# Performance work log

Measured on AMD Instinct MI355X. Metric: run time of the kernel, lower is better.

Reference implementation:

```python
import jax, jax.numpy as jnp
import numpy as np
import math

DIM = 512
HEADS = 16
HD = DIM // HEADS
HT, WT = 32, 32          # trained input_resolution
LT = HT * WT             # trained_len
TBL = (2 * HT - 1) * (2 * WT - 1)  # 3969 rows in relative_coords_table
CPB_HID = 512


def _l2norm(a, eps=1e-12):
    n = jnp.linalg.norm(a, axis=-1, keepdims=True)
    return a / jnp.maximum(n, eps)


def setup_inputs() -> dict:
    key = jax.random.key(0)
    ks = jax.random.split(key, 10)
    B, N = 8, 1024
    std = 0.02
    return {
        "x": jax.random.normal(ks[0], (B, N, DIM), jnp.float32),
        "qkv_w": jax.random.normal(ks[1], (3 * DIM, DIM), jnp.float32) * std,
        "qkv_b": jnp.zeros((3 * DIM,), jnp.float32),
        "proj_w": jax.random.normal(ks[2], (DIM, DIM), jnp.float32) * std,
        "proj_b": jnp.zeros((DIM,), jnp.float32),
        # softplus-inverse init: softplus(temperature) == 1/0.24
        "temperature": jnp.log(jnp.exp(jnp.ones((HEADS, 1, 1), jnp.float32) / 0.24) - 1.0),
        "query_embedding": jax.random.normal(ks[3], (HEADS, 1, HD), jnp.float32) * 0.02,
        "cpb_fc1_w": jax.random.normal(ks[4], (CPB_HID, 2), jnp.float32) * std,
        "cpb_fc1_b": jnp.zeros((CPB_HID,), jnp.float32),
        "cpb_fc2_w": jax.random.normal(ks[5], (HEADS, CPB_HID), jnp.float32) * std,
        "cpb_fc2_b": jnp.zeros((HEADS,), jnp.float32),
        "relative_coords_table": jax.random.uniform(ks[6], (TBL, 2), jnp.float32, -1.0, 1.0),
        "relative_pos_index": jax.random.randint(ks[7], (LT * LT,), 0, TBL, jnp.int32),
        "seq_length_scale": jnp.float32(math.log(float(N))),
        "padding_mask": jnp.zeros((B, N), bool),
        "H": 32,
        "W": 32,
    }


def reference(x, qkv_w, qkv_b, proj_w, proj_b, temperature, query_embedding,
              cpb_fc1_w, cpb_fc1_b, cpb_fc2_w, cpb_fc2_b,
              relative_coords_table, seq_length_scale,
              relative_pos_index, padding_mask, H, W):
    B, N, C = x.shape
    # qkv projection -> [B, N, 3, heads, hd] -> per-tensor [B, heads, N, hd]
    qkv = (x @ qkv_w.T + qkv_b).reshape(B, N, 3, HEADS, HD)
    q, k, v = (jnp.transpose(qkv[:, :, i], (0, 2, 1, 3)) for i in range(3))

    # continuous position bias MLP: [TBL, 2] -> [TBL, heads]
    t = jnp.maximum(relative_coords_table @ cpb_fc1_w.T + cpb_fc1_b, 0.0)
    t = t @ cpb_fc2_w.T + cpb_fc2_b                       # [TBL, heads]
    rb = t.T[:, relative_pos_index]                       # [heads, LT*LT]
    rb = rb.reshape(HEADS, LT, HT, WT)
    rb = jax.image.resize(rb, (HEADS, LT, H, W), 'bilinear')   # interp key axis
    rb = rb.reshape(HEADS, LT, N).transpose(0, 2, 1).reshape(HEADS, N, HT, WT)
    rb = jax.image.resize(rb, (HEADS, N, H, W), 'bilinear')    # interp query axis
    rb = rb.reshape(HEADS, N, N).transpose(0, 2, 1)             # [heads, N, N]

    scale = jax.nn.softplus(temperature) * seq_length_scale     # [heads, 1, 1]
    qn = (_l2norm(q) + query_embedding[None]) * scale[None]     # [B, heads, N, hd]
    kn = _l2norm(k)
    attn = jnp.einsum('bhnd,bhmd->bhnm', qn, kn) + rb[None]     # [B, heads, N, N]
    attn = jax.nn.softmax(attn, axis=-1)
    out = jnp.einsum('bhnm,bhmd->bhnd', attn, v)
    out = out.transpose(0, 2, 1, 3).reshape(B, N, C)
    return out @ proj_w.T + proj_b
```

## Files before the change

### kernel.cpp

```cpp
#include <hip/hip_runtime.h>
#include <math.h>

#define BATCH 8
#define NSEQ  1024
#define DIMC  512
#define HEADS 16
#define HD    32
#define TBLN  3969
#define QROWS (BATCH*HEADS*NSEQ)
#define LOG2E 1.4426950408889634f

typedef __attribute__((ext_vector_type(8))) short bf16x8;
typedef __attribute__((ext_vector_type(4))) float f32x4;

__device__ __forceinline__ unsigned short f2bf(float f) {
  union { float f; unsigned u; } c; c.f = f;
  unsigned x = c.u + 0x7fffu + ((c.u >> 16) & 1u);
  return (unsigned short)(x >> 16);
}
__device__ __forceinline__ float bf2f(unsigned short h) {
  union { unsigned u; float f; } c; c.u = ((unsigned)h) << 16; return c.f;
}
__device__ __forceinline__ unsigned cvt_pk_bf16(float lo, float hi) {
  unsigned r;
  asm("v_cvt_pk_bf16_f32 %0, %1, %2" : "=v"(r) : "v"(lo), "v"(hi));
  return r;
}

__global__ __launch_bounds__(256) void split_kernel(
    const float* __restrict__ src, unsigned short* __restrict__ hi,
    unsigned short* __restrict__ lo, int n4)
{
  int gid = blockIdx.x * 256 + threadIdx.x;
  if (gid >= n4) return;
  float4 v = ((const float4*)src)[gid];
  float vv[4] = {v.x, v.y, v.z, v.w};
  unsigned short h[4], l[4];
#pragma unroll
  for (int i = 0; i < 4; ++i) {
    h[i] = f2bf(vv[i]);
    l[i] = f2bf(vv[i] - bf2f(h[i]));
  }
  uint2 hp, lp;
  hp.x = h[0] | ((unsigned)h[1] << 16); hp.y = h[2] | ((unsigned)h[3] << 16);
  lp.x = l[0] | ((unsigned)l[1] << 16); lp.y = l[2] | ((unsigned)l[3] << 16);
  ((uint2*)hi)[gid] = hp;
  ((uint2*)lo)[gid] = lp;
}

template<int EPI>
__global__ __launch_bounds__(256) void gemm_split_kernel(
    const unsigned short* __restrict__ Ah, const unsigned short* __restrict__ Al,
    const unsigned short* __restrict__ Wh, const unsigned short* __restrict__ Wl,
    const float* __restrict__ bias,
    float* __restrict__ o0p, float* __restrict__ o1p, float* __restrict__ o2p)
{
  const int K = DIMC;
  __shared__ __align__(16) unsigned short lds[4 * 4096];
  unsigned short* ldsAh = lds;
  unsigned short* ldsAl = lds + 4096;
  unsigned short* ldsBh = lds + 8192;
  unsigned short* ldsBl = lds + 12288;
  const int tid = threadIdx.x;
  const int wave = tid >> 6, lane = tid & 63;
  const int l16 = lane & 15, hi4 = lane >> 4;
  const int rowBase = blockIdx.y * 128, colBase = blockIdx.x * 128;
  const int warpRow = (wave >> 1) * 64, warpCol = (wave & 1) * 64;

  const int o0 = wave * 2048 + lane * 16;
  const int o1 = o0 + 1024;
  const int row0 = o0 >> 6, s0 = (o0 >> 4) & 3;
  const int row1 = o1 >> 6, s1 = (o1 >> 4) & 3;
  const int g0 = row0 * K + ((s0 ^ ((row0 >> 1) & 3)) << 3);
  const int g1 = row1 * K + ((s1 ^ ((row1 >> 1) & 3)) << 3);

  const unsigned short* A0h = Ah + (size_t)rowBase * K;
  const unsigned short* A0l = Al + (size_t)rowBase * K;
  const unsigned short* W0h = Wh + (size_t)colBase * K;
  const unsigned short* W0l = Wl + (size_t)colBase * K;

  f32x4 acc[4][4] = {};

  float biasv[4];
#pragma unroll
  for (int fj = 0; fj < 4; ++fj)
    biasv[fj] = bias[colBase + warpCol + fj * 16 + l16];

  int ra[4], rbq[4];
#pragma unroll
  for (int f = 0; f < 4; ++f) {
    int rowA = warpRow + f * 16 + l16;
    ra[f] = rowA * 64 + ((hi4 ^ ((rowA >> 1) & 3)) << 4);
    int rowB = warpCol + f * 16 + l16;
    rbq[f] = rowB * 64 + ((hi4 ^ ((rowB >> 1) & 3)) << 4);
  }

#define GLD(gsrc, ldst) __builtin_amdgcn_global_load_lds( \
      (const __attribute__((address_space(1))) unsigned int*)(gsrc), \
      (__attribute__((address_space(3))) unsigned int*)(ldst), 16, 0, 0)

  for (int k0 = 0; k0 < K; k0 += 32) {
    __syncthreads();
    GLD(A0h + k0 + g0, (char*)ldsAh + o0);
    GLD(A0h + k0 + g1, (char*)ldsAh + o1);
    GLD(A0l + k0 + g0, (char*)ldsAl + o0);
    GLD(A0l + k0 + g1, (char*)ldsAl + o1);
    GLD(W0h + k0 + g0, (char*)ldsBh + o0);
    GLD(W0h + k0 + g1, (char*)ldsBh + o1);
    GLD(W0l + k0 + g0, (char*)ldsBl + o0);
    GLD(W0l + k0 + g1, (char*)ldsBl + o1);
    __syncthreads();

    bf16x8 a_h[4], a_l[4], b_h[4], b_l[4];
#pragma unroll
    for (int f = 0; f < 4; ++f) {
      a_h[f] = *(const bf16x8*)((const char*)ldsAh + ra[f]);
      a_l[f] = *(const bf16x8*)((const char*)ldsAl + ra[f]);
      b_h[f] = *(const bf16x8*)((const char*)ldsBh + rbq[f]);
      b_l[f] = *(const bf16x8*)((const char*)ldsBl + rbq[f]);
    }
#pragma unroll
    for (int fi = 0; fi < 4; ++fi)
#pragma unroll
      for (int fj = 0; fj < 4; ++fj) {
        acc[fi][fj] = __builtin_amdgcn_mfma_f32_16x16x32_bf16(a_l[fi], b_h[fj], acc[fi][fj], 0, 0, 0);
        acc[fi][fj] = __builtin_amdgcn_mfma_f32_16x16x32_bf16(a_h[fi], b_l[fj], acc[fi][fj], 0, 0, 0);
        acc[fi][fj] = __builtin_amdgcn_mfma_f32_16x16x32_bf16(a_h[fi], b_h[fj], acc[fi][fj], 0, 0, 0);
      }
  }
#undef GLD

#pragma unroll
  for (int fi = 0; fi < 4; ++fi)
#pragma unroll
    for (int fj = 0; fj < 4; ++fj)
#pragma unroll
      for (int r = 0; r < 4; ++r) {
        int m = rowBase + warpRow + fi * 16 + hi4 * 4 + r;
        int c = colBase + warpCol + fj * 16 + l16;
        float val = acc[fi][fj][r] + biasv[fj];
        if (EPI == 0) {
          int b = m >> 10, n = m & 1023;
          int which = c >> 9, rem = c & 511;
          int hh = rem >> 5, d = rem & 31;
          float* dst = (which == 0) ? o0p : (which == 1) ? o1p : o2p;
          dst[(((size_t)b * HEADS + hh) * NSEQ + n) * HD + d] = val;
        } else {
          o0p[(size_t)m * DIMC + c] = val;
        }
      }
}

__global__ __launch_bounds__(256) void cpb_kernel(
    const float* __restrict__ table, const float* __restrict__ fc1w,
    const float* __restrict__ fc1b, const float* __restrict__ fc2w,
    const float* __restrict__ fc2b, float* __restrict__ tT)
{
  const int row = blockIdx.x;
  const float c0 = table[row*2], c1 = table[row*2+1];
  __shared__ float hid[512];
  __shared__ float red[256];
  const int tid = threadIdx.x;
  for (int j = tid; j < 512; j += 256)
    hid[j] = fmaxf(fmaf(c0, fc1w[j*2], fmaf(c1, fc1w[j*2+1], fc1b[j])), 0.f);
  __syncthreads();
  const int h = tid & 15, part = tid >> 4;
  float s = 0.f;
#pragma unroll
  for (int jj = 0; jj < 32; ++jj) {
    int j = part*32 + jj;
    s = fmaf(hid[j], fc2w[h*512 + j], s);
  }
  red[tid] = s;
  __syncthreads();
  if (tid < 16) {
    float t = fc2b[tid];
#pragma unroll
    for (int p = 0; p < 16; ++p) t += red[tid + p*16];
    tT[(size_t)tid * TBLN + row] = t;
  }
}

__global__ __launch_bounds__(256) void rb_gather_kernel(
    const float* __restrict__ tT, const int* __restrict__ rpi,
    unsigned short* __restrict__ rb)
{
  int gid = blockIdx.x * 256 + threadIdx.x;
  int idx = rpi[gid];
#pragma unroll
  for (int h = 0; h < 16; ++h)
    rb[(size_t)h * NSEQ * NSEQ + gid] = f2bf(tT[h * TBLN + idx] * LOG2E);
}

__global__ __launch_bounds__(256) void rowmax_kernel(
    const unsigned short* __restrict__ rb, float* __restrict__ rbmax)
{
  const int row = blockIdx.x * 4 + (threadIdx.x >> 6);
  const int lane = threadIdx.x & 63;
  const unsigned short* src = rb + (size_t)row * NSEQ + lane * 16;
  bf16x8 a = *(const bf16x8*)src;
  bf16x8 b = *(const bf16x8*)(src + 8);
  float m = -1e30f;
#pragma unroll
  for (int j = 0; j < 8; ++j) {
    m = fmaxf(m, bf2f((unsigned short)a[j]));
    m = fmaxf(m, bf2f((unsigned short)b[j]));
  }
#pragma unroll
  for (int s = 32; s >= 1; s >>= 1) m = fmaxf(m, __shfl_xor(m, s));
  if (lane == 0) rbmax[row] = m;
}

__global__ __launch_bounds__(256) void normsplit_kernel(
    const float* __restrict__ qb, const float* __restrict__ kb,
    const float* __restrict__ temperature, const float* __restrict__ qe,
    const float* __restrict__ sls,
    unsigned short* __restrict__ qh, unsigned short* __restrict__ ql,
    unsigned short* __restrict__ kh, unsigned short* __restrict__ kl,
    float* __restrict__ qmag)
{
  const int gid = blockIdx.x * 256 + threadIdx.x;
  const int lane = gid & 31;
  const int row = gid >> 5;
  const bool isQ = row < QROWS;
  const float* src = isQ ? qb : kb;
  const int r = isQ ? row : row - QROWS;
  float x = src[(size_t)r * HD + lane];
  float ss = x * x;
#pragma unroll
  for (int m = 16; m >= 1; m >>= 1) ss += __shfl_xor(ss, m);
  float y = x / fmaxf(sqrtf(ss), 1e-12f);
  if (isQ) {
    const int h = (r >> 10) & (HEADS - 1);
    float scale = log1pf(__expf(temperature[h])) * sls[0];
    y = (y + qe[h * HD + lane]) * scale;
    float s2 = y * y;
#pragma unroll
    for (int m = 16; m >= 1; m >>= 1) s2 += __shfl_xor(s2, m);
    if (lane == 0) qmag[r] = sqrtf(s2);
  }
  unsigned short hi = f2bf(y);
  unsigned short lo = f2bf(y - bf2f(hi));
  size_t idx = (size_t)r * HD + lane;
  if (isQ) { qh[idx] = hi; ql[idx] = lo; }
  else     { kh[idx] = hi; kl[idx] = lo; }
}

__global__ __launch_bounds__(256) void vt_kernel(
    const float* __restrict__ vb, unsigned short* __restrict__ vt)
{
  __shared__ float tile[32][257];
  const int bh = blockIdx.x, ch = blockIdx.y;
  const int t = threadIdx.x;
  const float* src = vb + ((size_t)bh * NSEQ + ch * 256) * HD;
#pragma unroll
  for (int i = 0; i < 32; ++i) {
    int idx = i * 256 + t;
    tile[idx & 31][idx >> 5] = src[idx];
  }
  __syncthreads();
  unsigned short* dst = vt + (size_t)bh * HD * NSEQ + ch * 256;
#pragma unroll
  for (int i = 0; i < 32; ++i) {
    int idx = i * 256 + t;
    int d = idx >> 8, nl = idx & 255;
    dst[(size_t)d * NSEQ + nl] = f2bf(tile[d][nl]);
  }
}

__global__ __launch_bounds__(256, 4) void attn_mfma_kernel(
    const unsigned short* __restrict__ qh, const unsigned short* __restrict__ ql,
    const unsigned short* __restrict__ kh, const unsigned short* __restrict__ kl,
    const unsigned short* __restrict__ vt, const unsigned short* __restrict__ rb,
    const float* __restrict__ qmag, const float* __restrict__ rbmax,
    unsigned short* __restrict__ aoh, unsigned short* __restrict__ aol)
{
  const int bh = blockIdx.x;
  const int h = bh & (HEADS - 1), b = bh >> 4;
  const int wave = threadIdx.x >> 6;
  const int lane = threadIdx.x & 63;
  const int l16 = lane & 15, hi4 = lane >> 4;
  const int qbase = blockIdx.y * 128 + wave * 32;

  bf16x8 qhf[2], qlf[2];
  float Ms[2];
#pragma unroll
  for (int g = 0; g < 2; ++g) {
    const int qrow = qbase + g * 16 + l16;
    size_t ro = ((size_t)bh * NSEQ + qrow) * HD + hi4 * 8;
    qhf[g] = *(const bf16x8*)(qh + ro);
    qlf[g] = *(const bf16x8*)(ql + ro);
    Ms[g] = qmag[(size_t)bh * NSEQ + qrow] * (1.01f * LOG2E)
            + rbmax[h * NSEQ + qrow] + 0.2f;
  }

  bf16x8 ones;
#pragma unroll
  for (int j = 0; j < 8; ++j) ones[j] = (short)0x3f80;

  f32x4 accV[2][2] = {};
  f32x4 accL[2] = {};

  const int krow_p = 8 * (l16 >> 2) + (l16 & 3);

  for (int kt = 0; kt < NSEQ / 32; ++kt) {
    const int k0 = kt * 32;
    size_t kr0 = ((size_t)bh * NSEQ + k0 + krow_p) * HD + hi4 * 8;
    size_t kr1 = kr0 + 4 * HD;
    bf16x8 kh0 = *(const bf16x8*)(kh + kr0);
    bf16x8 kh1 = *(const bf16x8*)(kh + kr1);
    bf16x8 kl0 = *(const bf16x8*)(kl + kr0);
    bf16x8 kl1 = *(const bf16x8*)(kl + kr1);
    bf16x8 vt0 = *(const bf16x8*)(vt + ((size_t)bh * HD +  0 + l16) * NSEQ + k0 + hi4 * 8);
    bf16x8 vt1 = *(const bf16x8*)(vt + ((size_t)bh * HD + 16 + l16) * NSEQ + k0 + hi4 * 8);

#pragma unroll
    for (int g = 0; g < 2; ++g) {
      f32x4 D0 = {0.f, 0.f, 0.f, 0.f};
      f32x4 D1 = {0.f, 0.f, 0.f, 0.f};
      D0 = __builtin_amdgcn_mfma_f32_16x16x32_bf16(kh0, qhf[g], D0, 0, 0, 0);
      D0 = __builtin_amdgcn_mfma_f32_16x16x32_bf16(kh0, qlf[g], D0, 0, 0, 0);
      D0 = __builtin_amdgcn_mfma_f32_16x16x32_bf16(kl0, qhf[g], D0, 0, 0, 0);
      D1 = __builtin_amdgcn_mfma_f32_16x16x32_bf16(kh1, qhf[g], D1, 0, 0, 0);
      D1 = __builtin_amdgcn_mfma_f32_16x16x32_bf16(kh1, qlf[g], D1, 0, 0, 0);
      D1 = __builtin_amdgcn_mfma_f32_16x16x32_bf16(kl1, qhf[g], D1, 0, 0, 0);

      bf16x8 b8 = *(const bf16x8*)(rb + ((size_t)h * NSEQ + qbase + g * 16 + l16) * NSEQ + k0 + hi4 * 8);

      float p0[4], p1[4];
#pragma unroll
      for (int r = 0; r < 4; ++r) {
        float a0 = fmaf(D0[r], LOG2E, bf2f((unsigned short)b8[r]))     - Ms[g];
        float a1 = fmaf(D1[r], LOG2E, bf2f((unsigned short)b8[4 + r])) - Ms[g];
        p0[r] = __builtin_amdgcn_exp2f(a0);
        p1[r] = __builtin_amdgcn_exp2f(a1);
      }
      union { bf16x8 v; unsigned u[4]; } pa;
      pa.u[0] = cvt_pk_bf16(p0[0], p0[1]);
      pa.u[1] = cvt_pk_bf16(p0[2], p0[3]);
      pa.u[2] = cvt_pk_bf16(p1[0], p1[1]);
      pa.u[3] = cvt_pk_bf16(p1[2], p1[3]);

      accV[g][0] = __builtin_amdgcn_mfma_f32_16x16x32_bf16(pa.v, vt0, accV[g][0], 0, 0, 0);
      accV[g][1] = __builtin_amdgcn_mfma_f32_16x16x32_bf16(pa.v, vt1, accV[g][1], 0, 0, 0);
      accL[g]    = __builtin_amdgcn_mfma_f32_16x16x32_bf16(pa.v, ones, accL[g], 0, 0, 0);
    }
  }

#pragma unroll
  for (int g = 0; g < 2; ++g)
#pragma unroll
    for (int r = 0; r < 4; ++r) {
      float inv = 1.f / accL[g][r];
#pragma unroll
      for (int df = 0; df < 2; ++df) {
        size_t idx = ((size_t)b * NSEQ + qbase + g * 16 + hi4 * 4 + r) * DIMC
                     + h * HD + df * 16 + l16;
        float val = accV[g][df][r] * inv;
        unsigned short hh = f2bf(val);
        aoh[idx] = hh;
        aol[idx] = f2bf(val - bf2f(hh));
      }
    }
}

extern "C" void kernel_launch(void* const* d_in, const int* in_sizes, int n_in,
                              void* d_out, int out_size, void* d_ws, size_t ws_size,
                              hipStream_t stream)
{
  (void)in_sizes; (void)n_in; (void)out_size; (void)ws_size;
  const float* x      = (const float*)d_in[0];
  const float* qkv_w  = (const float*)d_in[1];
  const float* qkv_b  = (const float*)d_in[2];
  const float* proj_w = (const float*)d_in[3];
  const float* proj_b = (const float*)d_in[4];
  const float* temp   = (const float*)d_in[5];
  const float* qe     = (const float*)d_in[6];
  const float* fc1w   = (const float*)d_in[7];
  const float* fc1b   = (const float*)d_in[8];
  const float* fc2w   = (const float*)d_in[9];
  const float* fc2b   = (const float*)d_in[10];
  const float* tbl    = (const float*)d_in[11];
  const int*   rpi    = (const int*)d_in[12];
  const float* sls    = (const float*)d_in[13];

  char* ws = (char*)d_ws;
  const size_t perT = (size_t)BATCH * HEADS * NSEQ * HD;
  float* qb = (float*)ws;
  float* kb = qb + perT;
  float* vb = kb + perT;
  float* tT = vb + perT;
  unsigned short* qh = (unsigned short*)(tT + 65536);
  unsigned short* ql = qh + perT;
  unsigned short* kh = ql + perT;
  unsigned short* kl = kh + perT;
  unsigned short* vt = kl + perT;
  unsigned short* xh = vt + perT;
  unsigned short* xl = xh + perT;
  unsigned short* pwh = xl + perT;
  unsigned short* pwl = pwh + 262144;
  float* rbmax = (float*)(pwl + 262144);
  float* qmag  = rbmax + 16384;
  unsigned short* qwh = qh;
  unsigned short* qwl = qh + 786432;
  unsigned short* rb  = (unsigned short*)qb;
  unsigned short* aoh = xh;
  unsigned short* aol = xl;

  split_kernel<<<dim3(4096), 256, 0, stream>>>(x, xh, xl, 1048576);
  split_kernel<<<dim3(768),  256, 0, stream>>>(qkv_w, qwh, qwl, 196608);
  split_kernel<<<dim3(256),  256, 0, stream>>>(proj_w, pwh, pwl, 65536);
  gemm_split_kernel<0><<<dim3(12, 64), 256, 0, stream>>>(
      xh, xl, qwh, qwl, qkv_b, qb, kb, vb);
  cpb_kernel<<<dim3(TBLN), 256, 0, stream>>>(tbl, fc1w, fc1b, fc2w, fc2b, tT);
  normsplit_kernel<<<dim3((2*QROWS*32)/256), 256, 0, stream>>>(
      qb, kb, temp, qe, sls, qh, ql, kh, kl, qmag);
  vt_kernel<<<dim3(BATCH*HEADS, NSEQ/256), 256, 0, stream>>>(vb, vt);
  rb_gather_kernel<<<dim3((NSEQ*NSEQ)/256), 256, 0, stream>>>(tT, rpi, rb);
  rowmax_kernel<<<dim3(HEADS*NSEQ/4), 256, 0, stream>>>(rb, rbmax);
  attn_mfma_kernel<<<dim3(BATCH*HEADS, NSEQ/128), 256, 0, stream>>>(
      qh, ql, kh, kl, vt, rb, qmag, rbmax, aoh, aol);
  gemm_split_kernel<1><<<dim3(4, 64), 256, 0, stream>>>(
      aoh, aol, pwh, pwl, proj_b, (float*)d_out, nullptr, nullptr);
}
```

Before: 384.0 us.

## Double-buffer K/V/bias tile loads in registers and prioritize MFMA waves in attention

```diff
diff --git a/kernel.cpp b/kernel.cpp
--- a/kernel.cpp
+++ b/kernel.cpp
@@ -26,6 +26,10 @@
   asm("v_cvt_pk_bf16_f32 %0, %1, %2" : "=v"(r) : "v"(lo), "v"(hi));
   return r;
 }
+
+#define GLD(gsrc, ldst) __builtin_amdgcn_global_load_lds( \
+      (const __attribute__((address_space(1))) unsigned int*)(gsrc), \
+      (__attribute__((address_space(3))) unsigned int*)(ldst), 16, 0, 0)
 
 __global__ __launch_bounds__(256) void split_kernel(
     const float* __restrict__ src, unsigned short* __restrict__ hi,
@@ -95,10 +99,6 @@
     rbq[f] = rowB * 64 + ((hi4 ^ ((rowB >> 1) & 3)) << 4);
   }
 
-#define GLD(gsrc, ldst) __builtin_amdgcn_global_load_lds( \
-      (const __attribute__((address_space(1))) unsigned int*)(gsrc), \
-      (__attribute__((address_space(3))) unsigned int*)(ldst), 16, 0, 0)
-
   for (int k0 = 0; k0 < K; k0 += 32) {
     __syncthreads();
     GLD(A0h + k0 + g0, (char*)ldsAh + o0);
@@ -128,7 +128,6 @@
         acc[fi][fj] = __builtin_amdgcn_mfma_f32_16x16x32_bf16(a_h[fi], b_h[fj], acc[fi][fj], 0, 0, 0);
       }
   }
-#undef GLD
 
 #pragma unroll
   for (int fi = 0; fi < 4; ++fi)
@@ -268,7 +267,7 @@
   }
 }
 
-__global__ __launch_bounds__(256, 4) void attn_mfma_kernel(
+__global__ __launch_bounds__(256, 3) void attn_mfma_kernel(
     const unsigned short* __restrict__ qh, const unsigned short* __restrict__ ql,
     const unsigned short* __restrict__ kh, const unsigned short* __restrict__ kl,
     const unsigned short* __restrict__ vt, const unsigned short* __restrict__ rb,
@@ -302,50 +301,72 @@
   f32x4 accL[2] = {};
 
   const int krow_p = 8 * (l16 >> 2) + (l16 & 3);
-
-  for (int kt = 0; kt < NSEQ / 32; ++kt) {
-    const int k0 = kt * 32;
-    size_t kr0 = ((size_t)bh * NSEQ + k0 + krow_p) * HD + hi4 * 8;
-    size_t kr1 = kr0 + 4 * HD;
-    bf16x8 kh0 = *(const bf16x8*)(kh + kr0);
-    bf16x8 kh1 = *(const bf16x8*)(kh + kr1);
-    bf16x8 kl0 = *(const bf16x8*)(kl + kr0);
-    bf16x8 kl1 = *(const bf16x8*)(kl + kr1);
-    bf16x8 vt0 = *(const bf16x8*)(vt + ((size_t)bh * HD +  0 + l16) * NSEQ + k0 + hi4 * 8);
-    bf16x8 vt1 = *(const bf16x8*)(vt + ((size_t)bh * HD + 16 + l16) * NSEQ + k0 + hi4 * 8);
-
-#pragma unroll
-    for (int g = 0; g < 2; ++g) {
-      f32x4 D0 = {0.f, 0.f, 0.f, 0.f};
-      f32x4 D1 = {0.f, 0.f, 0.f, 0.f};
-      D0 = __builtin_amdgcn_mfma_f32_16x16x32_bf16(kh0, qhf[g], D0, 0, 0, 0);
-      D0 = __builtin_amdgcn_mfma_f32_16x16x32_bf16(kh0, qlf[g], D0, 0, 0, 0);
-      D0 = __builtin_amdgcn_mfma_f32_16x16x32_bf16(kl0, qhf[g], D0, 0, 0, 0);
-      D1 = __builtin_amdgcn_mfma_f32_16x16x32_bf16(kh1, qhf[g], D1, 0, 0, 0);
-      D1 = __builtin_amdgcn_mfma_f32_16x16x32_bf16(kh1, qlf[g], D1, 0, 0, 0);
-      D1 = __builtin_amdgcn_mfma_f32_16x16x32_bf16(kl1, qhf[g], D1, 0, 0, 0);
-
-      bf16x8 b8 = *(const bf16x8*)(rb + ((size_t)h * NSEQ + qbase + g * 16 + l16) * NSEQ + k0 + hi4 * 8);
-
-      float p0[4], p1[4];
-#pragma unroll
-      for (int r = 0; r < 4; ++r) {
-        float a0 = fmaf(D0[r], LOG2E, bf2f((unsigned short)b8[r]))     - Ms[g];
-        float a1 = fmaf(D1[r], LOG2E, bf2f((unsigned short)b8[4 + r])) - Ms[g];
-        p0[r] = __builtin_amdgcn_exp2f(a0);
-        p1[r] = __builtin_amdgcn_exp2f(a1);
-      }
-      union { bf16x8 v; unsigned u[4]; } pa;
-      pa.u[0] = cvt_pk_bf16(p0[0], p0[1]);
-      pa.u[1] = cvt_pk_bf16(p0[2], p0[3]);
-      pa.u[2] = cvt_pk_bf16(p1[0], p1[1]);
-      pa.u[3] = cvt_pk_bf16(p1[2], p1[3]);
-
-      accV[g][0] = __builtin_amdgcn_mfma_f32_16x16x32_bf16(pa.v, vt0, accV[g][0], 0, 0, 0);
-      accV[g][1] = __builtin_amdgcn_mfma_f32_16x16x32_bf16(pa.v, vt1, accV[g][1], 0, 0, 0);
-      accL[g]    = __builtin_amdgcn_mfma_f32_16x16x32_bf16(pa.v, ones, accL[g], 0, 0, 0);
-    }
-  }
+  const unsigned short* khg  = kh + ((size_t)bh * NSEQ + krow_p) * HD + hi4 * 8;
+  const unsigned short* klg  = kl + ((size_t)bh * NSEQ + krow_p) * HD + hi4 * 8;
+  const unsigned short* vtg  = vt + ((size_t)bh * HD + l16) * NSEQ + hi4 * 8;
+  const unsigned short* rbg0 = rb + ((size_t)h * NSEQ + qbase + l16) * NSEQ + hi4 * 8;
+  const unsigned short* rbg1 = rbg0 + (size_t)16 * NSEQ;
+
+#define LOADTILE(S, KT) do { \
+    const size_t ko_ = (size_t)(KT) * 32 * HD; \
+    const size_t vo_ = (size_t)(KT) * 32; \
+    kh0##S = *(const bf16x8*)(khg + ko_); \
+    kh1##S = *(const bf16x8*)(khg + ko_ + 4 * HD); \
+    kl0##S = *(const bf16x8*)(klg + ko_); \
+    kl1##S = *(const bf16x8*)(klg + ko_ + 4 * HD); \
+    vt0##S = *(const bf16x8*)(vtg + vo_); \
+    vt1##S = *(const bf16x8*)(vtg + vo_ + (size_t)16 * NSEQ); \
+    b80##S = *(const bf16x8*)(rbg0 + vo_); \
+    b81##S = *(const bf16x8*)(rbg1 + vo_); \
+  } while (0)
+
+#define COMPUTE(S) do { \
+    _Pragma("unroll") \
+    for (int g = 0; g < 2; ++g) { \
+      bf16x8 b8v = g ? b81##S : b80##S; \
+      f32x4 D0 = {0.f, 0.f, 0.f, 0.f}; \
+      f32x4 D1 = {0.f, 0.f, 0.f, 0.f}; \
+      __builtin_amdgcn_s_setprio(1); \
+      D0 = __builtin_amdgcn_mfma_f32_16x16x32_bf16(kh0##S, qhf[g], D0, 0, 0, 0); \
+      D0 = __builtin_amdgcn_mfma_f32_16x16x32_bf16(kh0##S, qlf[g], D0, 0, 0, 0); \
+      D0 = __builtin_amdgcn_mfma_f32_16x16x32_bf16(kl0##S, qhf[g], D0, 0, 0, 0); \
+      D1 = __builtin_amdgcn_mfma_f32_16x16x32_bf16(kh1##S, qhf[g], D1, 0, 0, 0); \
+      D1 = __builtin_amdgcn_mfma_f32_16x16x32_bf16(kh1##S, qlf[g], D1, 0, 0, 0); \
+      D1 = __builtin_amdgcn_mfma_f32_16x16x32_bf16(kl1##S, qhf[g], D1, 0, 0, 0); \
+      __builtin_amdgcn_s_setprio(0); \
+      float p0[4], p1[4]; \
+      _Pragma("unroll") \
+      for (int r = 0; r < 4; ++r) { \
+        float a0 = fmaf(D0[r], LOG2E, bf2f((unsigned short)b8v[r]))     - Ms[g]; \
+        float a1 = fmaf(D1[r], LOG2E, bf2f((unsigned short)b8v[4 + r])) - Ms[g]; \
+        p0[r] = __builtin_amdgcn_exp2f(a0); \
+        p1[r] = __builtin_amdgcn_exp2f(a1); \
+      } \
+      union { bf16x8 v; unsigned u[4]; } pa; \
+      pa.u[0] = cvt_pk_bf16(p0[0], p0[1]); \
+      pa.u[1] = cvt_pk_bf16(p0[2], p0[3]); \
+      pa.u[2] = cvt_pk_bf16(p1[0], p1[1]); \
+      pa.u[3] = cvt_pk_bf16(p1[2], p1[3]); \
+      __builtin_amdgcn_s_setprio(1); \
+      accV[g][0] = __builtin_amdgcn_mfma_f32_16x16x32_bf16(pa.v, vt0##S, accV[g][0], 0, 0, 0); \
+      accV[g][1] = __builtin_amdgcn_mfma_f32_16x16x32_bf16(pa.v, vt1##S, accV[g][1], 0, 0, 0); \
+      accL[g]    = __builtin_amdgcn_mfma_f32_16x16x32_bf16(pa.v, ones, accL[g], 0, 0, 0); \
+      __builtin_amdgcn_s_setprio(0); \
+    } \
+  } while (0)
+
+  bf16x8 kh0A, kh1A, kl0A, kl1A, vt0A, vt1A, b80A, b81A;
+  bf16x8 kh0B, kh1B, kl0B, kl1B, vt0B, vt1B, b80B, b81B;
+
+  LOADTILE(A, 0);
+  for (int kt = 0; kt < 32; kt += 2) {
+    LOADTILE(B, kt + 1);
+    COMPUTE(A);
+    LOADTILE(A, kt + 2);
+    COMPUTE(B);
+  }
+#undef LOADTILE
+#undef COMPUTE
 
 #pragma unroll
   for (int g = 0; g < 2; ++g)
```

New measurement: 388.1 us. About the same (+1.1%).

## Pre-swizzle K, V and bias into MFMA fragment layout for coalesced attention loads

Applied to the files above, without the earlier changes.

```diff
diff --git a/kernel.cpp b/kernel.cpp
--- a/kernel.cpp
+++ b/kernel.cpp
@@ -26,6 +26,10 @@
   asm("v_cvt_pk_bf16_f32 %0, %1, %2" : "=v"(r) : "v"(lo), "v"(hi));
   return r;
 }
+
+#define GLD(gsrc, ldst) __builtin_amdgcn_global_load_lds( \
+      (const __attribute__((address_space(1))) unsigned int*)(gsrc), \
+      (__attribute__((address_space(3))) unsigned int*)(ldst), 16, 0, 0)
 
 __global__ __launch_bounds__(256) void split_kernel(
     const float* __restrict__ src, unsigned short* __restrict__ hi,
@@ -95,10 +99,6 @@
     rbq[f] = rowB * 64 + ((hi4 ^ ((rowB >> 1) & 3)) << 4);
   }
 
-#define GLD(gsrc, ldst) __builtin_amdgcn_global_load_lds( \
-      (const __attribute__((address_space(1))) unsigned int*)(gsrc), \
-      (__attribute__((address_space(3))) unsigned int*)(ldst), 16, 0, 0)
-
   for (int k0 = 0; k0 < K; k0 += 32) {
     __syncthreads();
     GLD(A0h + k0 + g0, (char*)ldsAh + o0);
@@ -128,7 +128,6 @@
         acc[fi][fj] = __builtin_amdgcn_mfma_f32_16x16x32_bf16(a_h[fi], b_h[fj], acc[fi][fj], 0, 0, 0);
       }
   }
-#undef GLD
 
 #pragma unroll
   for (int fi = 0; fi < 4; ++fi)
@@ -183,23 +182,36 @@
 
 __global__ __launch_bounds__(256) void rb_gather_kernel(
     const float* __restrict__ tT, const int* __restrict__ rpi,
-    unsigned short* __restrict__ rb)
+    unsigned short* __restrict__ rbT)
 {
   int gid = blockIdx.x * 256 + threadIdx.x;
-  int idx = rpi[gid];
-#pragma unroll
-  for (int h = 0; h < 16; ++h)
-    rb[(size_t)h * NSEQ * NSEQ + gid] = f2bf(tT[h * TBLN + idx] * LOG2E);
+  int n = gid >> 7, m8 = gid & 127;
+  int idx[8];
+#pragma unroll
+  for (int j = 0; j < 8; ++j) idx[j] = rpi[(size_t)n * NSEQ + m8 * 8 + j];
+  const int kt = m8 >> 2, hi4v = m8 & 3;
+  const size_t base = (((size_t)0 * 64 + (n >> 4)) * 32 + kt) * 512
+                      + ((n & 15) + 16 * hi4v) * 8;
+#pragma unroll
+  for (int h = 0; h < 16; ++h) {
+    bf16x8 v;
+#pragma unroll
+    for (int j = 0; j < 8; ++j)
+      v[j] = (short)f2bf(tT[h * TBLN + idx[j]] * LOG2E);
+    *(bf16x8*)(rbT + base + (size_t)h * 64 * 32 * 512) = v;
+  }
 }
 
 __global__ __launch_bounds__(256) void rowmax_kernel(
-    const unsigned short* __restrict__ rb, float* __restrict__ rbmax)
+    const unsigned short* __restrict__ rbT, float* __restrict__ rbmax)
 {
   const int row = blockIdx.x * 4 + (threadIdx.x >> 6);
   const int lane = threadIdx.x & 63;
-  const unsigned short* src = rb + (size_t)row * NSEQ + lane * 16;
-  bf16x8 a = *(const bf16x8*)src;
-  bf16x8 b = *(const bf16x8*)(src + 8);
+  const int h = row >> 10, n = row & 1023;
+  const int kt = lane >> 1, half = lane & 1;
+  const size_t base = (((size_t)h * 64 + (n >> 4)) * 32 + kt) * 512;
+  bf16x8 a = *(const bf16x8*)(rbT + base + ((n & 15) + 16 * (2 * half)) * 8);
+  bf16x8 b = *(const bf16x8*)(rbT + base + ((n & 15) + 16 * (2 * half + 1)) * 8);
   float m = -1e30f;
 #pragma unroll
   for (int j = 0; j < 8; ++j) {
@@ -216,7 +228,7 @@
     const float* __restrict__ temperature, const float* __restrict__ qe,
     const float* __restrict__ sls,
     unsigned short* __restrict__ qh, unsigned short* __restrict__ ql,
-    unsigned short* __restrict__ kh, unsigned short* __restrict__ kl,
+    unsigned short* __restrict__ khT, unsigned short* __restrict__ klT,
     float* __restrict__ qmag)
 {
   const int gid = blockIdx.x * 256 + threadIdx.x;
@@ -241,13 +253,22 @@
   }
   unsigned short hi = f2bf(y);
   unsigned short lo = f2bf(y - bf2f(hi));
-  size_t idx = (size_t)r * HD + lane;
-  if (isQ) { qh[idx] = hi; ql[idx] = lo; }
-  else     { kh[idx] = hi; kl[idx] = lo; }
+  if (isQ) {
+    size_t idx = (size_t)r * HD + lane;
+    qh[idx] = hi; ql[idx] = lo;
+  } else {
+    const int bh = r >> 10, n = r & 1023;
+    const int kt = n >> 5, kr = n & 31;
+    const int s = (kr >> 2) & 1;
+    const int l16v = 4 * (kr >> 3) + (kr & 3);
+    size_t idx = ((((size_t)bh * 32 + kt) * 2 + s) * 512)
+                 + (l16v + 16 * (lane >> 3)) * 8 + (lane & 7);
+    khT[idx] = hi; klT[idx] = lo;
+  }
 }
 
 __global__ __launch_bounds__(256) void vt_kernel(
-    const float* __restrict__ vb, unsigned short* __restrict__ vt)
+    const float* __restrict__ vb, unsigned short* __restrict__ vtT)
 {
   __shared__ float tile[32][257];
   const int bh = blockIdx.x, ch = blockIdx.y;
@@ -259,19 +280,22 @@
     tile[idx & 31][idx >> 5] = src[idx];
   }
   __syncthreads();
-  unsigned short* dst = vt + (size_t)bh * HD * NSEQ + ch * 256;
+  unsigned short* dst = vtT + (size_t)bh * 32 * 2 * 512;
 #pragma unroll
   for (int i = 0; i < 32; ++i) {
     int idx = i * 256 + t;
     int d = idx >> 8, nl = idx & 255;
-    dst[(size_t)d * NSEQ + nl] = f2bf(tile[d][nl]);
-  }
-}
-
-__global__ __launch_bounds__(256, 4) void attn_mfma_kernel(
+    int n = ch * 256 + nl;
+    size_t a = (((size_t)(n >> 5) * 2) + (d >> 4)) * 512
+               + ((d & 15) + 16 * ((n >> 3) & 3)) * 8 + (n & 7);
+    dst[a] = f2bf(tile[d][nl]);
+  }
+}
+
+__global__ __launch_bounds__(256, 6) void attn_mfma_kernel(
     const unsigned short* __restrict__ qh, const unsigned short* __restrict__ ql,
-    const unsigned short* __restrict__ kh, const unsigned short* __restrict__ kl,
-    const unsigned short* __restrict__ vt, const unsigned short* __restrict__ rb,
+    const unsigned short* __restrict__ khT, const unsigned short* __restrict__ klT,
+    const unsigned short* __restrict__ vtT, const unsigned short* __restrict__ rbT,
     const float* __restrict__ qmag, const float* __restrict__ rbmax,
     unsigned short* __restrict__ aoh, unsigned short* __restrict__ aol)
 {
@@ -280,88 +304,84 @@
   const int wave = threadIdx.x >> 6;
   const int lane = threadIdx.x & 63;
   const int l16 = lane & 15, hi4 = lane >> 4;
-  const int qbase = blockIdx.y * 128 + wave * 32;
-
-  bf16x8 qhf[2], qlf[2];
-  float Ms[2];
-#pragma unroll
-  for (int g = 0; g < 2; ++g) {
-    const int qrow = qbase + g * 16 + l16;
+  const int qbase = blockIdx.y * 64 + wave * 16;
+
+  const int qrow = qbase + l16;
+  bf16x8 qhf, qlf;
+  {
     size_t ro = ((size_t)bh * NSEQ + qrow) * HD + hi4 * 8;
-    qhf[g] = *(const bf16x8*)(qh + ro);
-    qlf[g] = *(const bf16x8*)(ql + ro);
-    Ms[g] = qmag[(size_t)bh * NSEQ + qrow] * (1.01f * LOG2E)
-            + rbmax[h * NSEQ + qrow] + 0.2f;
-  }
+    qhf = *(const bf16x8*)(qh + ro);
+    qlf = *(const bf16x8*)(ql + ro);
+  }
+  const float Ms = qmag[(size_t)bh * NSEQ + qrow] * (1.01f * LOG2E)
+                   + rbmax[h * NSEQ + qrow] + 0.2f;
 
   bf16x8 ones;
 #pragma unroll
   for (int j = 0; j < 8; ++j) ones[j] = (short)0x3f80;
 
-  f32x4 accV[2][2] = {};
-  f32x4 accL[2] = {};
-
-  const int krow_p = 8 * (l16 >> 2) + (l16 & 3);
-
-  for (int kt = 0; kt < NSEQ / 32; ++kt) {
-    const int k0 = kt * 32;
-    size_t kr0 = ((size_t)bh * NSEQ + k0 + krow_p) * HD + hi4 * 8;
-    size_t kr1 = kr0 + 4 * HD;
-    bf16x8 kh0 = *(const bf16x8*)(kh + kr0);
-    bf16x8 kh1 = *(const bf16x8*)(kh + kr1);
-    bf16x8 kl0 = *(const bf16x8*)(kl + kr0);
-    bf16x8 kl1 = *(const bf16x8*)(kl + kr1);
-    bf16x8 vt0 = *(const bf16x8*)(vt + ((size_t)bh * HD +  0 + l16) * NSEQ + k0 + hi4 * 8);
-    bf16x8 vt1 = *(const bf16x8*)(vt + ((size_t)bh * HD + 16 + l16) * NSEQ + k0 + hi4 * 8);
-
-#pragma unroll
-    for (int g = 0; g < 2; ++g) {
-      f32x4 D0 = {0.f, 0.f, 0.f, 0.f};
-      f32x4 D1 = {0.f, 0.f, 0.f, 0.f};
-      D0 = __builtin_amdgcn_mfma_f32_16x16x32_bf16(kh0, qhf[g], D0, 0, 0, 0);
-      D0 = __builtin_amdgcn_mfma_f32_16x16x32_bf16(kh0, qlf[g], D0, 0, 0, 0);
-      D0 = __builtin_amdgcn_mfma_f32_16x16x32_bf16(kl0, qhf[g], D0, 0, 0, 0);
-      D1 = __builtin_amdgcn_mfma_f32_16x16x32_bf16(kh1, qhf[g], D1, 0, 0, 0);
-      D1 = __builtin_amdgcn_mfma_f32_16x16x32_bf16(kh1, qlf[g], D1, 0, 0, 0);
-      D1 = __builtin_amdgcn_mfma_f32_16x16x32_bf16(kl1, qhf[g], D1, 0, 0, 0);
-
-      bf16x8 b8 = *(const bf16x8*)(rb + ((size_t)h * NSEQ + qbase + g * 16 + l16) * NSEQ + k0 + hi4 * 8);
-
-      float p0[4], p1[4];
-#pragma unroll
-      for (int r = 0; r < 4; ++r) {
-        float a0 = fmaf(D0[r], LOG2E, bf2f((unsigned short)b8[r]))     - Ms[g];
-        float a1 = fmaf(D1[r], LOG2E, bf2f((unsigned short)b8[4 + r])) - Ms[g];
-        p0[r] = __builtin_amdgcn_exp2f(a0);
-        p1[r] = __builtin_amdgcn_exp2f(a1);
-      }
-      union { bf16x8 v; unsigned u[4]; } pa;
-      pa.u[0] = cvt_pk_bf16(p0[0], p0[1]);
-      pa.u[1] = cvt_pk_bf16(p0[2], p0[3]);
-      pa.u[2] = cvt_pk_bf16(p1[0], p1[1]);
-      pa.u[3] = cvt_pk_bf16(p1[2], p1[3]);
-
-      accV[g][0] = __builtin_amdgcn_mfma_f32_16x16x32_bf16(pa.v, vt0, accV[g][0], 0, 0, 0);
-      accV[g][1] = __builtin_amdgcn_mfma_f32_16x16x32_bf16(pa.v, vt1, accV[g][1], 0, 0, 0);
-      accL[g]    = __builtin_amdgcn_mfma_f32_16x16x32_bf16(pa.v, ones, accL[g], 0, 0, 0);
+  f32x4 accV0 = {}, accV1 = {}, accL = {};
+
+  const unsigned short* khB = khT + (size_t)bh * 32768 + lane * 8;
+  const unsigned short* klB = klT + (size_t)bh * 32768 + lane * 8;
+  const unsigned short* vtB = vtT + (size_t)bh * 32768 + lane * 8;
+  const unsigned short* rbB = rbT
+      + ((size_t)(h * 64 + blockIdx.y * 4 + wave) * 32) * 512 + lane * 8;
+
+  for (int kt = 0; kt < 32; ++kt) {
+    bf16x8 kh0 = *(const bf16x8*)(khB + kt * 1024);
+    bf16x8 kh1 = *(const bf16x8*)(khB + kt * 1024 + 512);
+    bf16x8 kl0 = *(const bf16x8*)(klB + kt * 1024);
+    bf16x8 kl1 = *(const bf16x8*)(klB + kt * 1024 + 512);
+    bf16x8 vt0 = *(const bf16x8*)(vtB + kt * 1024);
+    bf16x8 vt1 = *(const bf16x8*)(vtB + kt * 1024 + 512);
+    bf16x8 b8  = *(const bf16x8*)(rbB + kt * 512);
+
+    f32x4 D0 = {0.f, 0.f, 0.f, 0.f};
+    f32x4 D1 = {0.f, 0.f, 0.f, 0.f};
+    __builtin_amdgcn_s_setprio(1);
+    D0 = __builtin_amdgcn_mfma_f32_16x16x32_bf16(kh0, qhf, D0, 0, 0, 0);
+    D0 = __builtin_amdgcn_mfma_f32_16x16x32_bf16(kh0, qlf, D0, 0, 0, 0);
+    D0 = __builtin_amdgcn_mfma_f32_16x16x32_bf16(kl0, qhf, D0, 0, 0, 0);
+    D1 = __builtin_amdgcn_mfma_f32_16x16x32_bf16(kh1, qhf, D1, 0, 0, 0);
+    D1 = __builtin_amdgcn_mfma_f32_16x16x32_bf16(kh1, qlf, D1, 0, 0, 0);
+    D1 = __builtin_amdgcn_mfma_f32_16x16x32_bf16(kl1, qhf, D1, 0, 0, 0);
+    __builtin_amdgcn_s_setprio(0);
+
+    float p0[4], p1[4];
+#pragma unroll
+    for (int r = 0; r < 4; ++r) {
+      float a0 = fmaf(D0[r], LOG2E, bf2f((unsigned short)b8[r]))     - Ms;
+      float a1 = fmaf(D1[r], LOG2E, bf2f((unsigned short)b8[4 + r])) - Ms;
+      p0[r] = __builtin_amdgcn_exp2f(a0);
+      p1[r] = __builtin_amdgcn_exp2f(a1);
     }
-  }
-
-#pragma unroll
-  for (int g = 0; g < 2; ++g)
-#pragma unroll
-    for (int r = 0; r < 4; ++r) {
-      float inv = 1.f / accL[g][r];
-#pragma unroll
-      for (int df = 0; df < 2; ++df) {
-        size_t idx = ((size_t)b * NSEQ + qbase + g * 16 + hi4 * 4 + r) * DIMC
-                     + h * HD + df * 16 + l16;
-        float val = accV[g][df][r] * inv;
-        unsigned short hh = f2bf(val);
-        aoh[idx] = hh;
-        aol[idx] = f2bf(val - bf2f(hh));
-      }
+    union { bf16x8 v; unsigned u[4]; } pa;
+    pa.u[0] = cvt_pk_bf16(p0[0], p0[1]);
+    pa.u[1] = cvt_pk_bf16(p0[2], p0[3]);
+    pa.u[2] = cvt_pk_bf16(p1[0], p1[1]);
+    pa.u[3] = cvt_pk_bf16(p1[2], p1[3]);
+
+    __builtin_amdgcn_s_setprio(1);
+    accV0 = __builtin_amdgcn_mfma_f32_16x16x32_bf16(pa.v, vt0, accV0, 0, 0, 0);
+    accV1 = __builtin_amdgcn_mfma_f32_16x16x32_bf16(pa.v, vt1, accV1, 0, 0, 0);
+    accL  = __builtin_amdgcn_mfma_f32_16x16x32_bf16(pa.v, ones, accL, 0, 0, 0);
+    __builtin_amdgcn_s_setprio(0);
+  }
+
+#pragma unroll
+  for (int r = 0; r < 4; ++r) {
+    float inv = 1.f / accL[r];
+#pragma unroll
+    for (int df = 0; df < 2; ++df) {
+      size_t idx = ((size_t)b * NSEQ + qbase + hi4 * 4 + r) * DIMC
+                   + h * HD + df * 16 + l16;
+      float val = (df ? accV1[r] : accV0[r]) * inv;
+      unsigned short hh = f2bf(val);
+      aoh[idx] = hh;
+      aol[idx] = f2bf(val - bf2f(hh));
     }
+  }
 }
 
 extern "C" void kernel_launch(void* const* d_in, const int* in_sizes, int n_in,
@@ -392,10 +412,10 @@
   float* tT = vb + perT;
   unsigned short* qh = (unsigned short*)(tT + 65536);
   unsigned short* ql = qh + perT;
-  unsigned short* kh = ql + perT;
-  unsigned short* kl = kh + perT;
-  unsigned short* vt = kl + perT;
-  unsigned short* xh = vt + perT;
+  unsigned short* khT = ql + perT;
+  unsigned short* klT = khT + perT;
+  unsigned short* vtT = klT + perT;
+  unsigned short* xh = vtT + perT;
   unsigned short* xl = xh + perT;
   unsigned short* pwh = xl + perT;
   unsigned short* pwl = pwh + 262144;
@@ -403,7 +423,7 @@
   float* qmag  = rbmax + 16384;
   unsigned short* qwh = qh;
   unsigned short* qwl = qh + 786432;
-  unsigned short* rb  = (unsigned short*)qb;
+  unsigned short* rbT = (unsigned short*)qb;
   unsigned short* aoh = xh;
   unsigned short* aol = xl;
 
@@ -414,12 +434,12 @@
       xh, xl, qwh, qwl, qkv_b, qb, kb, vb);
   cpb_kernel<<<dim3(TBLN), 256, 0, stream>>>(tbl, fc1w, fc1b, fc2w, fc2b, tT);
   normsplit_kernel<<<dim3((2*QROWS*32)/256), 256, 0, stream>>>(
-      qb, kb, temp, qe, sls, qh, ql, kh, kl, qmag);
-  vt_kernel<<<dim3(BATCH*HEADS, NSEQ/256), 256, 0, stream>>>(vb, vt);
-  rb_gather_kernel<<<dim3((NSEQ*NSEQ)/256), 256, 0, stream>>>(tT, rpi, rb);
-  rowmax_kernel<<<dim3(HEADS*NSEQ/4), 256, 0, stream>>>(rb, rbmax);
-  attn_mfma_kernel<<<dim3(BATCH*HEADS, NSEQ/128), 256, 0, stream>>>(
-      qh, ql, kh, kl, vt, rb, qmag, rbmax, aoh, aol);
+      qb, kb, temp, qe, sls, qh, ql, khT, klT, qmag);
+  vt_kernel<<<dim3(BATCH*HEADS, NSEQ/256), 256, 0, stream>>>(vb, vtT);
+  rb_gather_kernel<<<dim3((NSEQ*NSEQ/8)/256), 256, 0, stream>>>(tT, rpi, rbT);
+  rowmax_kernel<<<dim3(HEADS*NSEQ/4), 256, 0, stream>>>(rbT, rbmax);
+  attn_mfma_kernel<<<dim3(BATCH*HEADS, NSEQ/64), 256, 0, stream>>>(
+      qh, ql, khT, klT, vtT, rbT, qmag, rbmax, aoh, aol);
   gemm_split_kernel<1><<<dim3(4, 64), 256, 0, stream>>>(
       aoh, aol, pwh, pwl, proj_b, (float*)d_out, nullptr, nullptr);
 }
```

Result: faster. 353.7 us (-7.9%).
